# Kernel optimization log

Measured on AMD Instinct MI355X. Metric: run time of the kernel, lower is better.

The kernel has to match this reference:

```python
import jax, jax.numpy as jnp
import numpy as np

N_NODES = 100000

def gcn_conv(x, W, b, src, dst, n):
    # PyG GCNConv with add_self_loops=True, symmetric normalization.
    # Transform first (reduces feature dim before irregular aggregation).
    h = x @ W  # [N, out]
    # degree with self loops: in-degree over dst plus 1 per node
    deg = jax.ops.segment_sum(jnp.ones_like(dst, dtype=h.dtype), dst, num_segments=n) + 1.0
    dinv = jax.lax.rsqrt(deg)  # deg >= 1 due to self loops
    norm = dinv[src] * dinv[dst]  # [E]
    # message = norm * h[src], aggregated at dst; self-loop term = dinv_i^2 * h_i
    agg = jax.ops.segment_sum(h[src] * norm[:, None], dst, num_segments=n)
    agg = agg + h * (dinv * dinv)[:, None]
    return agg + b

def setup_inputs() -> dict:
    key = jax.random.key(0)
    k1, k2, k3, k4, k5 = jax.random.split(key, 5)
    F_in, H, E_dim = 128, 64, 64
    node_features = jax.random.normal(k1, (N_NODES, F_in), dtype=jnp.float32)
    edge_index = jax.random.randint(k2, (2, 1600000), 0, N_NODES, dtype=jnp.int64)
    s = 1.0 / np.sqrt(F_in)
    W1 = jax.random.uniform(k3, (F_in, H), jnp.float32, -s, s)
    b1 = jnp.zeros((H,), jnp.float32)
    s2 = 1.0 / np.sqrt(H)
    W2 = jax.random.uniform(k4, (H, H), jnp.float32, -s2, s2)
    b2 = jnp.zeros((H,), jnp.float32)
    Wl = jax.random.uniform(k5, (H, E_dim), jnp.float32, -s2, s2)
    bl = jnp.zeros((E_dim,), jnp.float32)
    return {"node_features": node_features, "edge_index": edge_index,
            "W1": W1, "b1": b1, "W2": W2, "b2": b2, "Wl": Wl, "bl": bl}

def reference(node_features, edge_index, W1, b1, W2, b2, Wl, bl):
    src, dst = edge_index[0], edge_index[1]
    n = node_features.shape[0]
    x = node_features.astype(jnp.float32)
    x = jax.nn.relu(gcn_conv(x, W1, b1, src, dst, n))
    # dropout: train=False -> identity
    x = jax.nn.relu(gcn_conv(x, W2, b2, src, dst, n))
    x = x @ Wl + bl
    return jax.nn.sigmoid(x).T  # [embed_size, N]
```

## Files before the change

### kernel.cpp

```cpp
#include <hip/hip_runtime.h>
#include <hip/hip_bf16.h>


#define FEAT 64
#define FIN 128
#define PAD 64
#define CAP 4608
#define EPB 4096
#define MAXNB 512

typedef __attribute__((ext_vector_type(8))) short  short8;
typedef __attribute__((ext_vector_type(4))) float  f32x4;

__device__ __forceinline__ unsigned short f2bf(float f) {
    union { float f; unsigned u; } x; x.f = f;
    unsigned r = x.u + 0x7FFF + ((x.u >> 16) & 1);
    return (unsigned short)(r >> 16);
}
__device__ __forceinline__ float bflo(unsigned u) {
    union { unsigned v; float f; } x; x.v = u << 16; return x.f;
}
__device__ __forceinline__ float bfhi(unsigned u) {
    union { unsigned v; float f; } x; x.v = u & 0xFFFF0000u; return x.f;
}

__global__ void wtrans_kernel(const float* __restrict__ W1, const float* __restrict__ W2,
                              const float* __restrict__ Wl,
                              unsigned short* __restrict__ Wt1, unsigned short* __restrict__ Wt2,
                              unsigned short* __restrict__ Wlt, int* __restrict__ bcnt) {
    int t = blockIdx.x * 256 + threadIdx.x;
    if (t < FIN * 64) {
        int k = t >> 6, n = t & 63;
        Wt1[n * FIN + k] = f2bf(W1[t]);
    } else if (t < FIN * 64 + 64 * 64) {
        int u = t - FIN * 64;
        int k = u >> 6, n = u & 63;
        Wt2[n * 64 + k] = f2bf(W2[u]);
    } else if (t < FIN * 64 + 2 * 64 * 64) {
        int u = t - FIN * 64 - 64 * 64;
        int k = u >> 6, n = u & 63;
        Wlt[n * 64 + k] = f2bf(Wl[u]);
    } else if (t < FIN * 64 + 2 * 64 * 64 + MAXNB * 16) {
        bcnt[t - FIN * 64 - 2 * 64 * 64] = 0;
    }
}

__global__ __launch_bounds__(256) void bin_kernel(const int* __restrict__ ei,
                                                  int* __restrict__ bcnt,
                                                  int* __restrict__ bbuf,
                                                  int E, int nb) {
    __shared__ int hist[MAXNB];
    __shared__ int base[MAXNB];
    __shared__ int cur[MAXNB];
    for (int t = threadIdx.x; t < nb; t += 256) { hist[t] = 0; cur[t] = 0; }
    __syncthreads();
    int e0 = blockIdx.x * EPB;
    int sreg[16], dreg[16];
#pragma unroll
    for (int k = 0; k < 16; ++k) {
        int idx = e0 + k * 256 + threadIdx.x;
        if (idx < E) {
            sreg[k] = ei[idx];
            dreg[k] = ei[E + idx];
            atomicAdd(&hist[dreg[k] >> 8], 1);
        } else {
            dreg[k] = -1;
        }
    }
    __syncthreads();
    for (int t = threadIdx.x; t < nb; t += 256) {
        int h = hist[t];
        base[t] = (h > 0) ? atomicAdd(&bcnt[t * 16], h) : 0;
    }
    __syncthreads();
#pragma unroll
    for (int k = 0; k < 16; ++k) {
        if (dreg[k] >= 0) {
            int b = dreg[k] >> 8;
            int p = base[b] + atomicAdd(&cur[b], 1);
            if (p < CAP)
                bbuf[(size_t)b * CAP + p] = sreg[k] | ((dreg[k] & 255) << 20);
        }
    }
}

__global__ __launch_bounds__(256) void ell_from_bins_kernel(const int* __restrict__ bbuf,
                                                            const int* __restrict__ bcnt,
                                                            int* __restrict__ col,
                                                            int* __restrict__ cnt,
                                                            float* __restrict__ dinv,
                                                            unsigned int* __restrict__ gz,
                                                            int N) {
    __shared__ int lcnt[256];
    int b = blockIdx.x;
    int d0 = b << 8;
    lcnt[threadIdx.x] = 0;
    if (b == 0 && threadIdx.x < 32)
        gz[(size_t)N * 32 + threadIdx.x] = 0u;
    __syncthreads();
    int ne = bcnt[b * 16];
    if (ne > CAP) ne = CAP;
    const int* eb = bbuf + (size_t)b * CAP;
    for (int i = threadIdx.x; i < ne; i += 256) {
        int w = eb[i];
        int s = w & 0xFFFFF;
        int dl = w >> 20;
        int slot = atomicAdd(&lcnt[dl], 1);
        if (slot < PAD) col[(size_t)(d0 + dl) * PAD + slot] = s;
    }
    __syncthreads();
    int d = d0 + threadIdx.x;
    if (d < N) {
        int c = lcnt[threadIdx.x];
        if (c > PAD) c = PAD;
        int c8 = (c + 7) & ~7;
        for (int k = c; k < c8; ++k) col[(size_t)d * PAD + k] = N;
        cnt[d] = c;
        dinv[d] = rsqrtf((float)c + 1.0f);
    }
}

__global__ __launch_bounds__(256) void gemm1_mfma_kernel(const float* __restrict__ x,
                                                         const unsigned short* __restrict__ Wt,
                                                         const float* __restrict__ dinv,
                                                         unsigned short* __restrict__ g, int N) {
    const int lane = threadIdx.x & 63;
    const int wave = threadIdx.x >> 6;
    const int m = lane & 15, quad = lane >> 4;
    const int r0 = blockIdx.x * 64 + wave * 16;
    const int arow = r0 + m;
    const bool aok = arow < N;
    f32x4 acc[4] = {f32x4{0,0,0,0}, f32x4{0,0,0,0}, f32x4{0,0,0,0}, f32x4{0,0,0,0}};
    union { short8 s; unsigned short u[8]; } a;
#pragma unroll
    for (int s = 0; s < FIN / 32; ++s) {
        if (aok) {
            const float* xp = x + (size_t)arow * FIN + s * 32 + quad * 8;
            float4 a0 = *(const float4*)xp;
            float4 a1 = *(const float4*)(xp + 4);
            a.u[0] = f2bf(a0.x); a.u[1] = f2bf(a0.y);
            a.u[2] = f2bf(a0.z); a.u[3] = f2bf(a0.w);
            a.u[4] = f2bf(a1.x); a.u[5] = f2bf(a1.y);
            a.u[6] = f2bf(a1.z); a.u[7] = f2bf(a1.w);
        } else {
#pragma unroll
            for (int k = 0; k < 8; ++k) a.u[k] = 0;
        }
#pragma unroll
        for (int t = 0; t < 4; ++t) {
            const unsigned short* bp = Wt + (size_t)(t * 16 + m) * FIN + s * 32 + quad * 8;
            short8 bf = *(const short8*)bp;
            acc[t] = __builtin_amdgcn_mfma_f32_16x16x32_bf16(a.s, bf, acc[t], 0, 0, 0);
        }
    }
    const int rbase = r0 + quad * 4;
#pragma unroll
    for (int i = 0; i < 4; ++i) {
        int r = rbase + i;
        if (r < N) {
            float di = dinv[r];
#pragma unroll
            for (int t = 0; t < 4; ++t)
                g[(size_t)r * 64 + t * 16 + m] = f2bf(di * acc[t][i]);
        }
    }
}

__global__ __launch_bounds__(256) void gemm2_mfma_kernel(const unsigned short* __restrict__ xb,
                                                         const unsigned short* __restrict__ Wt,
                                                         const float* __restrict__ dinv,
                                                         unsigned short* __restrict__ g, int N) {
    const int lane = threadIdx.x & 63;
    const int wave = threadIdx.x >> 6;
    const int m = lane & 15, quad = lane >> 4;
    const int r0 = blockIdx.x * 64 + wave * 16;
    const int arow = r0 + m;
    const bool aok = arow < N;
    f32x4 acc[4] = {f32x4{0,0,0,0}, f32x4{0,0,0,0}, f32x4{0,0,0,0}, f32x4{0,0,0,0}};
    const short8 zero8 = short8{0,0,0,0,0,0,0,0};
#pragma unroll
    for (int s = 0; s < 2; ++s) {
        short8 a = aok ? *(const short8*)(xb + (size_t)arow * 64 + s * 32 + quad * 8) : zero8;
#pragma unroll
        for (int t = 0; t < 4; ++t) {
            short8 bf = *(const short8*)(Wt + (size_t)(t * 16 + m) * 64 + s * 32 + quad * 8);
            acc[t] = __builtin_amdgcn_mfma_f32_16x16x32_bf16(a, bf, acc[t], 0, 0, 0);
        }
    }
    const int rbase = r0 + quad * 4;
#pragma unroll
    for (int i = 0; i < 4; ++i) {
        int r = rbase + i;
        if (r < N) {
            float di = dinv[r];
#pragma unroll
            for (int t = 0; t < 4; ++t)
                g[(size_t)r * 64 + t * 16 + m] = f2bf(di * acc[t][i]);
        }
    }
}

__global__ __launch_bounds__(256) void agg_relu_kernel(const unsigned short* __restrict__ g,
                                                       const int* __restrict__ cnt,
                                                       const int* __restrict__ col,
                                                       const float* __restrict__ dinv,
                                                       const float* __restrict__ b,
                                                       unsigned short* __restrict__ xout, int N) {
    int node = blockIdx.x * 4 + (threadIdx.x >> 6);
    if (node >= N) return;
    int lane = threadIdx.x & 63;
    int rg = lane >> 3, fc = lane & 7;
    int c = cnt[node];
    if (c > PAD) c = PAD;
    int c8 = (c + 7) & ~7;
    const int* cl = col + (size_t)node * PAD;
    float acc[8] = {0.f, 0.f, 0.f, 0.f, 0.f, 0.f, 0.f, 0.f};
#pragma unroll 2
    for (int j = 0; j < c8; j += 8) {
        int s = cl[j + rg];
        uint4 w = *(const uint4*)(g + (size_t)s * 64 + fc * 8);
        acc[0] += bflo(w.x); acc[1] += bfhi(w.x);
        acc[2] += bflo(w.y); acc[3] += bfhi(w.y);
        acc[4] += bflo(w.z); acc[5] += bfhi(w.z);
        acc[6] += bflo(w.w); acc[7] += bfhi(w.w);
    }
#pragma unroll
    for (int mk = 8; mk <= 32; mk <<= 1)
#pragma unroll
        for (int k = 0; k < 8; ++k)
            acc[k] += __shfl_xor(acc[k], mk, 64);
    if (rg == 0) {
        uint4 w = *(const uint4*)(g + (size_t)node * 64 + fc * 8);
        acc[0] += bflo(w.x); acc[1] += bfhi(w.x);
        acc[2] += bflo(w.y); acc[3] += bfhi(w.y);
        acc[4] += bflo(w.z); acc[5] += bfhi(w.z);
        acc[6] += bflo(w.w); acc[7] += bfhi(w.w);
        float di = dinv[node];
        float4 b0 = *(const float4*)&b[fc * 8];
        float4 b1 = *(const float4*)&b[fc * 8 + 4];
        union { uint4 v; unsigned short u[8]; } o;
        o.u[0] = f2bf(fmaxf(di * acc[0] + b0.x, 0.f));
        o.u[1] = f2bf(fmaxf(di * acc[1] + b0.y, 0.f));
        o.u[2] = f2bf(fmaxf(di * acc[2] + b0.z, 0.f));
        o.u[3] = f2bf(fmaxf(di * acc[3] + b0.w, 0.f));
        o.u[4] = f2bf(fmaxf(di * acc[4] + b1.x, 0.f));
        o.u[5] = f2bf(fmaxf(di * acc[5] + b1.y, 0.f));
        o.u[6] = f2bf(fmaxf(di * acc[6] + b1.z, 0.f));
        o.u[7] = f2bf(fmaxf(di * acc[7] + b1.w, 0.f));
        *(uint4*)&xout[(size_t)node * 64 + fc * 8] = o.v;
    }
}

__global__ __launch_bounds__(256) void final_mfma_kernel(const unsigned short* __restrict__ x2,
                                                         const unsigned short* __restrict__ Wlt,
                                                         const float* __restrict__ bl,
                                                         float* __restrict__ out, int N) {
    const int lane = threadIdx.x & 63;
    const int wave = threadIdx.x >> 6;
    const int m = lane & 15, quad = lane >> 4;
    const int r0 = blockIdx.x * 64 + wave * 16;
    const int arow = r0 + m;
    const bool aok = arow < N;
    f32x4 acc[4] = {f32x4{0,0,0,0}, f32x4{0,0,0,0}, f32x4{0,0,0,0}, f32x4{0,0,0,0}};
    const short8 zero8 = short8{0,0,0,0,0,0,0,0};
#pragma unroll
    for (int s = 0; s < 2; ++s) {
        short8 a = aok ? *(const short8*)(x2 + (size_t)arow * 64 + s * 32 + quad * 8) : zero8;
#pragma unroll
        for (int t = 0; t < 4; ++t) {
            short8 bf = *(const short8*)(Wlt + (size_t)(t * 16 + m) * 64 + s * 32 + quad * 8);
            acc[t] = __builtin_amdgcn_mfma_f32_16x16x32_bf16(a, bf, acc[t], 0, 0, 0);
        }
    }
    const int rbase = r0 + quad * 4;
    if (rbase + 3 < N && (N & 3) == 0) {
#pragma unroll
        for (int t = 0; t < 4; ++t) {
            int j = t * 16 + m;
            float bj = bl[j];
            float4 o;
            o.x = 1.f / (1.f + __expf(-(acc[t][0] + bj)));
            o.y = 1.f / (1.f + __expf(-(acc[t][1] + bj)));
            o.z = 1.f / (1.f + __expf(-(acc[t][2] + bj)));
            o.w = 1.f / (1.f + __expf(-(acc[t][3] + bj)));
            *(float4*)&out[(size_t)j * N + rbase] = o;
        }
    } else {
#pragma unroll
        for (int t = 0; t < 4; ++t) {
            int j = t * 16 + m;
            float bj = bl[j];
#pragma unroll
            for (int i = 0; i < 4; ++i) {
                int r = rbase + i;
                if (r < N)
                    out[(size_t)j * N + r] = 1.f / (1.f + __expf(-(acc[t][i] + bj)));
            }
        }
    }
}

extern "C" void kernel_launch(void* const* d_in, const int* in_sizes, int n_in,
                              void* d_out, int out_size, void* d_ws, size_t ws_size,
                              hipStream_t stream) {
    const float* x   = (const float*)d_in[0];
    const int*   ei  = (const int*)d_in[1];
    const float* W1  = (const float*)d_in[2];
    const float* b1  = (const float*)d_in[3];
    const float* W2  = (const float*)d_in[4];
    const float* b2  = (const float*)d_in[5];
    const float* Wl  = (const float*)d_in[6];
    const float* bl  = (const float*)d_in[7];
    float*       out = (float*)d_out;

    int N  = in_sizes[0] / FIN;
    int E  = in_sizes[1] / 2;
    int nb = (N + 255) >> 8;
    int ng = (N + 63) >> 6;

    int*            bcnt = (int*)d_ws;
    unsigned short* Wt1  = (unsigned short*)(bcnt + MAXNB * 16);
    unsigned short* Wt2  = Wt1 + FIN * 64;
    unsigned short* Wlt  = Wt2 + 64 * 64;
    int*            cnt  = (int*)(Wlt + 64 * 64);
    float*          dinv = (float*)(cnt + N);
    int*            col  = (int*)(dinv + N);
    int*            bbuf = col + (size_t)N * PAD;
    unsigned short* bufG = (unsigned short*)bbuf;
    unsigned short* bufX = bufG + (size_t)(N + 1) * FEAT;

    int wtot = FIN * 64 + 2 * 64 * 64 + MAXNB * 16;
    wtrans_kernel<<<(wtot + 255) / 256, 256, 0, stream>>>(W1, W2, Wl, Wt1, Wt2, Wlt, bcnt);

    bin_kernel<<<(E + EPB - 1) / EPB, 256, 0, stream>>>(ei, bcnt, bbuf, E, nb);
    ell_from_bins_kernel<<<nb, 256, 0, stream>>>(bbuf, bcnt, col, cnt, dinv,
                                                 (unsigned int*)bufG, N);

    gemm1_mfma_kernel<<<ng, 256, 0, stream>>>(x, Wt1, dinv, bufG, N);
    agg_relu_kernel<<<(N + 3) / 4, 256, 0, stream>>>(bufG, cnt, col, dinv, b1, bufX, N);

    gemm2_mfma_kernel<<<ng, 256, 0, stream>>>(bufX, Wt2, dinv, bufG, N);
    agg_relu_kernel<<<(N + 3) / 4, 256, 0, stream>>>(bufG, cnt, col, dinv, b2, bufX, N);

    final_mfma_kernel<<<ng, 256, 0, stream>>>(bufX, Wlt, bl, out, N);
}
```

Before: 275.4 us.

## Map eight nodes per wave in aggregation and reuse histogram atomics for binning

The aggregation kernel now assigns eight lanes per node, so each wave handles eight nodes instead of one. This removes the cross-lane shuffle reduction, and each lane walks its node's neighbour list four at a time using packed float2 adds, with padding indices pointing at a zero row N. The binning kernel reuses the return value of the shared histogram atomic as the slot offset, which drops the second atomic pass, and halves edges per block. The trade-off is divergence: each wave loops to the largest degree among its eight nodes, and column-index loads are no longer coalesced across lanes.

```diff
diff --git a/kernel.cpp b/kernel.cpp
--- a/kernel.cpp
+++ b/kernel.cpp
@@ -6,11 +6,12 @@
 #define FIN 128
 #define PAD 64
 #define CAP 4608
-#define EPB 4096
+#define EPB 2048
 #define MAXNB 512
 
 typedef __attribute__((ext_vector_type(8))) short  short8;
 typedef __attribute__((ext_vector_type(4))) float  f32x4;
+typedef __attribute__((ext_vector_type(2))) float  float2v;
 
 __device__ __forceinline__ unsigned short f2bf(float f) {
     union { float f; unsigned u; } x; x.f = f;
@@ -51,18 +52,17 @@
                                                   int E, int nb) {
     __shared__ int hist[MAXNB];
     __shared__ int base[MAXNB];
-    __shared__ int cur[MAXNB];
-    for (int t = threadIdx.x; t < nb; t += 256) { hist[t] = 0; cur[t] = 0; }
+    for (int t = threadIdx.x; t < nb; t += 256) hist[t] = 0;
     __syncthreads();
     int e0 = blockIdx.x * EPB;
-    int sreg[16], dreg[16];
-#pragma unroll
-    for (int k = 0; k < 16; ++k) {
+    int sreg[8], dreg[8], preg[8];
+#pragma unroll
+    for (int k = 0; k < 8; ++k) {
         int idx = e0 + k * 256 + threadIdx.x;
         if (idx < E) {
             sreg[k] = ei[idx];
             dreg[k] = ei[E + idx];
-            atomicAdd(&hist[dreg[k] >> 8], 1);
+            preg[k] = atomicAdd(&hist[dreg[k] >> 8], 1);
         } else {
             dreg[k] = -1;
         }
@@ -74,10 +74,10 @@
     }
     __syncthreads();
 #pragma unroll
-    for (int k = 0; k < 16; ++k) {
+    for (int k = 0; k < 8; ++k) {
         if (dreg[k] >= 0) {
             int b = dreg[k] >> 8;
-            int p = base[b] + atomicAdd(&cur[b], 1);
+            int p = base[b] + preg[k];
             if (p < CAP)
                 bbuf[(size_t)b * CAP + p] = sreg[k] | ((dreg[k] & 255) << 20);
         }
@@ -206,47 +206,72 @@
                                                        const float* __restrict__ dinv,
                                                        const float* __restrict__ b,
                                                        unsigned short* __restrict__ xout, int N) {
-    int node = blockIdx.x * 4 + (threadIdx.x >> 6);
-    if (node >= N) return;
-    int lane = threadIdx.x & 63;
-    int rg = lane >> 3, fc = lane & 7;
-    int c = cnt[node];
-    if (c > PAD) c = PAD;
-    int c8 = (c + 7) & ~7;
+    const int lane = threadIdx.x & 63;
+    const int wave = threadIdx.x >> 6;
+    const int ng = lane >> 3, fc = lane & 7;
+    const int node = blockIdx.x * 32 + wave * 8 + ng;
+    const bool valid = node < N;
+    int c8 = 0;
+    if (valid) {
+        int c = cnt[node];
+        if (c > PAD) c = PAD;
+        c8 = (c + 7) & ~7;
+    }
+    int cmax = c8;
+#pragma unroll
+    for (int mk = 8; mk <= 32; mk <<= 1) {
+        int o = __shfl_xor(cmax, mk, 64);
+        cmax = cmax > o ? cmax : o;
+    }
     const int* cl = col + (size_t)node * PAD;
-    float acc[8] = {0.f, 0.f, 0.f, 0.f, 0.f, 0.f, 0.f, 0.f};
-#pragma unroll 2
-    for (int j = 0; j < c8; j += 8) {
-        int s = cl[j + rg];
-        uint4 w = *(const uint4*)(g + (size_t)s * 64 + fc * 8);
-        acc[0] += bflo(w.x); acc[1] += bfhi(w.x);
-        acc[2] += bflo(w.y); acc[3] += bfhi(w.y);
-        acc[4] += bflo(w.z); acc[5] += bfhi(w.z);
-        acc[6] += bflo(w.w); acc[7] += bfhi(w.w);
-    }
-#pragma unroll
-    for (int mk = 8; mk <= 32; mk <<= 1)
-#pragma unroll
-        for (int k = 0; k < 8; ++k)
-            acc[k] += __shfl_xor(acc[k], mk, 64);
-    if (rg == 0) {
-        uint4 w = *(const uint4*)(g + (size_t)node * 64 + fc * 8);
-        acc[0] += bflo(w.x); acc[1] += bfhi(w.x);
-        acc[2] += bflo(w.y); acc[3] += bfhi(w.y);
-        acc[4] += bflo(w.z); acc[5] += bfhi(w.z);
-        acc[6] += bflo(w.w); acc[7] += bfhi(w.w);
+    float2v acc0 = {0.f, 0.f}, acc1 = {0.f, 0.f}, acc2 = {0.f, 0.f}, acc3 = {0.f, 0.f};
+    {
+        uint4 w = *(const uint4*)(g + (size_t)(valid ? node : N) * 64 + fc * 8);
+        acc0 += (float2v){bflo(w.x), bfhi(w.x)};
+        acc1 += (float2v){bflo(w.y), bfhi(w.y)};
+        acc2 += (float2v){bflo(w.z), bfhi(w.z)};
+        acc3 += (float2v){bflo(w.w), bfhi(w.w)};
+    }
+    for (int j = 0; j < cmax; j += 4) {
+        bool ok = j < c8;
+        int s0 = ok ? cl[j]     : N;
+        int s1 = ok ? cl[j + 1] : N;
+        int s2 = ok ? cl[j + 2] : N;
+        int s3 = ok ? cl[j + 3] : N;
+        uint4 w0 = *(const uint4*)(g + (size_t)s0 * 64 + fc * 8);
+        uint4 w1 = *(const uint4*)(g + (size_t)s1 * 64 + fc * 8);
+        uint4 w2 = *(const uint4*)(g + (size_t)s2 * 64 + fc * 8);
+        uint4 w3 = *(const uint4*)(g + (size_t)s3 * 64 + fc * 8);
+        acc0 += (float2v){bflo(w0.x), bfhi(w0.x)};
+        acc1 += (float2v){bflo(w0.y), bfhi(w0.y)};
+        acc2 += (float2v){bflo(w0.z), bfhi(w0.z)};
+        acc3 += (float2v){bflo(w0.w), bfhi(w0.w)};
+        acc0 += (float2v){bflo(w1.x), bfhi(w1.x)};
+        acc1 += (float2v){bflo(w1.y), bfhi(w1.y)};
+        acc2 += (float2v){bflo(w1.z), bfhi(w1.z)};
+        acc3 += (float2v){bflo(w1.w), bfhi(w1.w)};
+        acc0 += (float2v){bflo(w2.x), bfhi(w2.x)};
+        acc1 += (float2v){bflo(w2.y), bfhi(w2.y)};
+        acc2 += (float2v){bflo(w2.z), bfhi(w2.z)};
+        acc3 += (float2v){bflo(w2.w), bfhi(w2.w)};
+        acc0 += (float2v){bflo(w3.x), bfhi(w3.x)};
+        acc1 += (float2v){bflo(w3.y), bfhi(w3.y)};
+        acc2 += (float2v){bflo(w3.z), bfhi(w3.z)};
+        acc3 += (float2v){bflo(w3.w), bfhi(w3.w)};
+    }
+    if (valid) {
         float di = dinv[node];
         float4 b0 = *(const float4*)&b[fc * 8];
         float4 b1 = *(const float4*)&b[fc * 8 + 4];
         union { uint4 v; unsigned short u[8]; } o;
-        o.u[0] = f2bf(fmaxf(di * acc[0] + b0.x, 0.f));
-        o.u[1] = f2bf(fmaxf(di * acc[1] + b0.y, 0.f));
-        o.u[2] = f2bf(fmaxf(di * acc[2] + b0.z, 0.f));
-        o.u[3] = f2bf(fmaxf(di * acc[3] + b0.w, 0.f));
-        o.u[4] = f2bf(fmaxf(di * acc[4] + b1.x, 0.f));
-        o.u[5] = f2bf(fmaxf(di * acc[5] + b1.y, 0.f));
-        o.u[6] = f2bf(fmaxf(di * acc[6] + b1.z, 0.f));
-        o.u[7] = f2bf(fmaxf(di * acc[7] + b1.w, 0.f));
+        o.u[0] = f2bf(fmaxf(di * acc0.x + b0.x, 0.f));
+        o.u[1] = f2bf(fmaxf(di * acc0.y + b0.y, 0.f));
+        o.u[2] = f2bf(fmaxf(di * acc1.x + b0.z, 0.f));
+        o.u[3] = f2bf(fmaxf(di * acc1.y + b0.w, 0.f));
+        o.u[4] = f2bf(fmaxf(di * acc2.x + b1.x, 0.f));
+        o.u[5] = f2bf(fmaxf(di * acc2.y + b1.y, 0.f));
+        o.u[6] = f2bf(fmaxf(di * acc3.x + b1.z, 0.f));
+        o.u[7] = f2bf(fmaxf(di * acc3.y + b1.w, 0.f));
         *(uint4*)&xout[(size_t)node * 64 + fc * 8] = o.v;
     }
 }
@@ -337,10 +362,10 @@
                                                  (unsigned int*)bufG, N);
 
     gemm1_mfma_kernel<<<ng, 256, 0, stream>>>(x, Wt1, dinv, bufG, N);
-    agg_relu_kernel<<<(N + 3) / 4, 256, 0, stream>>>(bufG, cnt, col, dinv, b1, bufX, N);
+    agg_relu_kernel<<<(N + 31) / 32, 256, 0, stream>>>(bufG, cnt, col, dinv, b1, bufX, N);
 
     gemm2_mfma_kernel<<<ng, 256, 0, stream>>>(bufX, Wt2, dinv, bufG, N);
-    agg_relu_kernel<<<(N + 3) / 4, 256, 0, stream>>>(bufG, cnt, col, dinv, b2, bufX, N);
+    agg_relu_kernel<<<(N + 31) / 32, 256, 0, stream>>>(bufG, cnt, col, dinv, b2, bufX, N);
 
     final_mfma_kernel<<<ng, 256, 0, stream>>>(bufX, Wlt, bl, out, N);
 }
```

After: 266.7 us. 1.03x faster.
